# Kernel optimization log

Hardware: AMD Instinct MI355X
Metric: run time of the kernel (lower is better)

The kernel has to match this reference:

```python
import jax, jax.numpy as jnp
import numpy as np

D_MODEL = 1024
NUM_HEADS = 16
D_K = D_MODEL // NUM_HEADS
B, L = 2, 2048
NEG = -1e9


def setup_inputs() -> dict:
    key = jax.random.key(0)
    ks = jax.random.split(key, 11)
    s = 1.0 / np.sqrt(D_MODEL)
    inp = {
        "Q": jax.random.normal(ks[0], (B, L, D_MODEL), jnp.float32),
        "K": jax.random.normal(ks[1], (B, L, D_MODEL), jnp.float32),
        "V": jax.random.normal(ks[2], (B, L, D_MODEL), jnp.float32),
        # causal mask: True = valid (attend), False = masked
        "mask": jnp.tril(jnp.ones((L, L), bool))[None, None],
        # torch nn.Linear weights stored [out, in]
        "Wq": jax.random.normal(ks[3], (D_MODEL, D_MODEL), jnp.float32) * s,
        "bq": jnp.zeros((D_MODEL,), jnp.float32),
        "Wk": jax.random.normal(ks[4], (D_MODEL, D_MODEL), jnp.float32) * s,
        "bk": jnp.zeros((D_MODEL,), jnp.float32),
        "Wv": jax.random.normal(ks[5], (D_MODEL, D_MODEL), jnp.float32) * s,
        "bv": jnp.zeros((D_MODEL,), jnp.float32),
        "Wo": jax.random.normal(ks[6], (D_MODEL, D_MODEL), jnp.float32) * s,
        "bo": jnp.zeros((D_MODEL,), jnp.float32),
    }
    return inp


def _split_heads(x):  # [B,L,D] -> [B,H,L,d_k]
    b, l, _ = x.shape
    return x.reshape(b, l, NUM_HEADS, D_K).transpose(0, 2, 1, 3)


def reference(Q, K, V, mask, Wq, bq, Wk, bk, Wv, bv, Wo, bo):
    # linear projections (torch Linear: x @ W.T + b)
    q = _split_heads(Q @ Wq.T + bq)
    k = _split_heads(K @ Wk.T + bk)
    v = _split_heads(V @ Wv.T + bv)
    scores = jnp.einsum("bhqd,bhkd->bhqk", q, k) / jnp.sqrt(jnp.float32(D_K))
    scores = jnp.where(mask, scores, NEG)
    probs = jax.nn.softmax(scores, axis=-1)  # dropout inactive at inference
    attn = jnp.einsum("bhqk,bhkd->bhqd", probs, v)
    b, h, l, dk = attn.shape
    o_in = attn.transpose(0, 2, 1, 3).reshape(b, l, D_MODEL)
    return o_in @ Wo.T + bo
```

## Files before the change

kernel.cpp:

```cpp
#include <hip/hip_runtime.h>
#include <stdint.h>

#define D_MODEL 1024
#define NH 16
#define DK 64
#define BBATCH 2
#define LL 2048
#define SCALE_LOG2E 0.1803368801111244f

typedef unsigned short bfu;
typedef __attribute__((ext_vector_type(8))) short bf16x8;
typedef __attribute__((ext_vector_type(4))) float f32x4;

union BF8 { uint32_t w[4]; bf16x8 v; };

__device__ __forceinline__ bfu f2bf(float f) {
    union { float f; uint32_t u; } a; a.f = f;
    uint32_t r = a.u + 0x7FFF + ((a.u >> 16) & 1);
    return (bfu)(r >> 16);
}
__device__ __forceinline__ uint32_t pktrunc(float hi, float lo) {
    return __builtin_amdgcn_perm(__float_as_uint(hi), __float_as_uint(lo), 0x07060302);
}

__device__ __forceinline__ void gload_lds16(const void* g, void* l) {
    __builtin_amdgcn_global_load_lds(
        (const __attribute__((address_space(1))) void*)g,
        (__attribute__((address_space(3))) void*)l, 16, 0, 0);
}

__global__ __launch_bounds__(256) void cvt_all(
    const float4* __restrict__ s0, const float4* __restrict__ s1, const float4* __restrict__ s2,
    const float4* __restrict__ s3, const float4* __restrict__ s4, const float4* __restrict__ s5,
    const float4* __restrict__ s6, ushort4* __restrict__ dst)
{
    int i = blockIdx.x * 256 + threadIdx.x;
    const float4* s; int off;
    float sc = 1.0f;
    if (i < (3 << 20)) {
        int t = i >> 20; s = (t == 0) ? s0 : ((t == 1) ? s1 : s2);
        off = i & ((1 << 20) - 1);
    } else {
        int j = i - (3 << 20);
        int t = j >> 18; s = (t == 0) ? s3 : ((t == 1) ? s4 : ((t == 2) ? s5 : s6));
        if (t == 0) sc = SCALE_LOG2E;
        off = j & ((1 << 18) - 1);
    }
    float4 v = s[off];
    ushort4 o;
    o.x = f2bf(v.x * sc); o.y = f2bf(v.y * sc); o.z = f2bf(v.z * sc); o.w = f2bf(v.w * sc);
    dst[i] = o;
}

#define BM 128
#define BN 128
#define BKK 64

__device__ __forceinline__ int kperm(int k) {
    return (((k >> 4) & 1) << 5) | (((k >> 2) & 3) << 3) | (((k >> 5) & 1) << 2) | (k & 3);
}

__global__ __launch_bounds__(256, 2) void gemm_proj(
    const bfu* __restrict__ Qb, const bfu* __restrict__ Kb, const bfu* __restrict__ Vb,
    const bfu* __restrict__ Wq, const bfu* __restrict__ Wk, const bfu* __restrict__ Wv,
    const float* __restrict__ bq, const float* __restrict__ bk, const float* __restrict__ bv,
    bfu* __restrict__ qp, bfu* __restrict__ kp, bfu* __restrict__ vt)
{
    const int z = blockIdx.z;
    const bfu* A = (z == 0) ? Qb : ((z == 1) ? Kb : Vb);
    const bfu* B = (z == 0) ? Wq : ((z == 1) ? Wk : Wv);
    const float* bias = (z == 0) ? bq : ((z == 1) ? bk : bv);
    const float bsc = (z == 0) ? SCALE_LOG2E : 1.0f;
    bfu* out = (z == 0) ? qp : ((z == 1) ? kp : vt);

    __shared__ __align__(16) bfu As[BM * BKK];
    __shared__ __align__(16) bfu Bs[BN * BKK];

    const int t = threadIdx.x;
    const int lane = t & 63;
    const int wave = t >> 6;
    const int wm = wave & 1, wn = wave >> 1;
    const int tm = blockIdx.y * BM, tn = blockIdx.x * BN;
    const int lr = lane & 15, quad = lane >> 4, q8 = quad << 3;

    f32x4 acc[4][4];
    for (int i = 0; i < 4; i++) for (int j = 0; j < 4; j++) acc[i][j] = (f32x4){0.f, 0.f, 0.f, 0.f};

    for (int kt = 0; kt < 1024; kt += BKK) {
        for (int it = 0; it < 4; ++it) {
            int c = t + it * 256;
            int row = c >> 3, col = (c & 7) << 3;
            gload_lds16(&A[(size_t)(tm + row) * 1024 + kt + col], &As[(size_t)c * 8]);
        }
        for (int it = 0; it < 4; ++it) {
            int c = t + it * 256;
            int row = c >> 3, col = (c & 7) << 3;
            gload_lds16(&B[(size_t)(tn + row) * 1024 + kt + col], &Bs[(size_t)c * 8]);
        }
        __syncthreads();
        for (int ks = 0; ks < BKK; ks += 32) {
            bf16x8 a[4], b[4];
            for (int i = 0; i < 4; i++)
                a[i] = *(const bf16x8*)&As[(wm * 64 + i * 16 + lr) * BKK + ks + q8];
            for (int i = 0; i < 4; i++)
                b[i] = *(const bf16x8*)&Bs[(wn * 64 + i * 16 + lr) * BKK + ks + q8];
            for (int mt = 0; mt < 4; mt++)
                for (int nt = 0; nt < 4; nt++)
                    acc[mt][nt] = __builtin_amdgcn_mfma_f32_16x16x32_bf16(a[mt], b[nt], acc[mt][nt], 0, 0, 0);
        }
        __syncthreads();
    }

    for (int mt = 0; mt < 4; mt++)
        for (int nt = 0; nt < 4; nt++)
            for (int r = 0; r < 4; r++) {
                int m = tm + wm * 64 + mt * 16 + quad * 4 + r;
                int n = tn + wn * 64 + nt * 16 + lr;
                float v = acc[mt][nt][r] + bias[n] * bsc;
                int b_ = m >> 11, l = m & 2047;
                int h = n >> 6, d = n & 63;
                if (z < 2)
                    out[((size_t)((b_ * NH + h) * LL + l)) * DK + d] = f2bf(v);
                else {
                    int lp = (l & ~63) | kperm(l & 63);
                    out[((size_t)((b_ * NH + h) * DK + d)) * LL + lp] = f2bf(v);
                }
            }
}

__global__ __launch_bounds__(256) void attn_kernel(
    const bfu* __restrict__ qp, const bfu* __restrict__ kp, const bfu* __restrict__ vtp,
    bfu* __restrict__ attn)
{
    const int id = blockIdx.x;
    const int bh = (id & 7) | ((id >> 7) << 3);
    const int band = 15 - ((id >> 3) & 15);
    const int b_ = bh >> 4, h = bh & 15;
    const int t = threadIdx.x;
    const int lane = t & 63, w = t >> 6;
    const int lr = lane & 15, quad = lane >> 4, q8 = quad << 3;

    __shared__ __align__(16) bfu Ks[2][64 * 64];
    __shared__ __align__(16) bfu Vs[2][64 * 64];

    const int r0 = band * 128 + w * 32;
    const int jmax_b = 2 * band + 1;
    const int jmax_w = r0 >> 6;

    const bfu* kbase = kp + (size_t)bh * LL * DK;
    const bfu* vbase = vtp + (size_t)bh * DK * LL;

    bf16x8 aq[2][2];
    for (int mt = 0; mt < 2; mt++)
        for (int kx = 0; kx < 2; kx++)
            aq[mt][kx] = *(const bf16x8*)&qp[((size_t)bh * LL + r0 + mt * 16 + lr) * DK + kx * 32 + q8];

    f32x4 o[2][4];
    for (int mt = 0; mt < 2; mt++)
        for (int nf = 0; nf < 4; nf++) o[mt][nf] = (f32x4){0.f, 0.f, 0.f, 0.f};
    float lsum[2] = {0.f, 0.f};

    {
        for (int it = 0; it < 2; ++it) {
            int c = t + it * 256;
            gload_lds16(&kbase[(size_t)(0 * 64 + (c >> 3)) * DK + (c & 7) * 8], &Ks[0][(size_t)c * 8]);
        }
        for (int it = 0; it < 2; ++it) {
            int c = t + it * 256;
            gload_lds16(&vbase[(size_t)(c >> 3) * LL + 0 * 64 + (c & 7) * 8], &Vs[0][(size_t)c * 8]);
        }
    }
    __syncthreads();

    for (int j = 0; j <= jmax_b; ++j) {
        const int buf = j & 1;
        if (j < jmax_b) {
            const int nb = buf ^ 1, jn = j + 1;
            for (int it = 0; it < 2; ++it) {
                int c = t + it * 256;
                gload_lds16(&kbase[(size_t)(jn * 64 + (c >> 3)) * DK + (c & 7) * 8], &Ks[nb][(size_t)c * 8]);
            }
            for (int it = 0; it < 2; ++it) {
                int c = t + it * 256;
                gload_lds16(&vbase[(size_t)(c >> 3) * LL + jn * 64 + (c & 7) * 8], &Vs[nb][(size_t)c * 8]);
            }
        }
        if (j <= jmax_w) {
            f32x4 sv[4][2];
            for (int kt = 0; kt < 4; kt++)
                for (int mt = 0; mt < 2; mt++) sv[kt][mt] = (f32x4){0.f, 0.f, 0.f, 0.f};
            for (int kx = 0; kx < 2; kx++)
                for (int kt = 0; kt < 4; kt++) {
                    bf16x8 ak = *(const bf16x8*)&Ks[buf][(kt * 16 + lr) * 64 + kx * 32 + q8];
                    for (int mt = 0; mt < 2; mt++)
                        sv[kt][mt] = __builtin_amdgcn_mfma_f32_16x16x32_bf16(ak, aq[mt][kx], sv[kt][mt], 0, 0, 0);
                }
            if (j == jmax_w) {
                const int mb = r0 & 63;
                for (int kt = 0; kt < 4; kt++)
                    for (int mt = 0; mt < 2; mt++)
                        for (int r = 0; r < 4; r++) {
                            int kl = kt * 16 + quad * 4 + r;
                            int ml = mb + mt * 16 + lr;
                            if (kl > ml) sv[kt][mt][r] = -1e9f;
                        }
            }
            for (int kt = 0; kt < 4; kt++)
                for (int mt = 0; mt < 2; mt++)
                    for (int r = 0; r < 4; r++) {
                        float e = __builtin_amdgcn_exp2f(sv[kt][mt][r]);
                        sv[kt][mt][r] = e;
                        lsum[mt] += e;
                    }
            for (int kx = 0; kx < 2; kx++) {
                BF8 pf[2];
                for (int mt = 0; mt < 2; mt++) {
                    pf[mt].w[0] = pktrunc(sv[kx][mt][1], sv[kx][mt][0]);
                    pf[mt].w[1] = pktrunc(sv[kx][mt][3], sv[kx][mt][2]);
                    pf[mt].w[2] = pktrunc(sv[2 + kx][mt][1], sv[2 + kx][mt][0]);
                    pf[mt].w[3] = pktrunc(sv[2 + kx][mt][3], sv[2 + kx][mt][2]);
                }
                for (int nf = 0; nf < 4; nf++) {
                    bf16x8 av = *(const bf16x8*)&Vs[buf][(nf * 16 + lr) * 64 + kx * 32 + q8];
                    for (int mt = 0; mt < 2; mt++)
                        o[mt][nf] = __builtin_amdgcn_mfma_f32_16x16x32_bf16(av, pf[mt].v, o[mt][nf], 0, 0, 0);
                }
            }
        }
        __syncthreads();
    }

    for (int mt = 0; mt < 2; mt++) {
        float l = lsum[mt];
        l += __shfl_xor(l, 16);
        l += __shfl_xor(l, 32);
        float rinv = 1.0f / l;
        for (int nf = 0; nf < 4; nf++) {
            uint32_t w0 = ((uint32_t)f2bf(o[mt][nf][1] * rinv) << 16) | f2bf(o[mt][nf][0] * rinv);
            uint32_t w1 = ((uint32_t)f2bf(o[mt][nf][3] * rinv) << 16) | f2bf(o[mt][nf][2] * rinv);
            uint2 pk2 = {w0, w1};
            *(uint2*)&attn[((size_t)(b_ * LL + r0 + mt * 16 + lr)) * D_MODEL + h * DK + nf * 16 + quad * 4] = pk2;
        }
    }
}

#define OBM 128
#define OBN 64

__global__ __launch_bounds__(256) void gemm_out(
    const bfu* __restrict__ A, const bfu* __restrict__ B,
    const float* __restrict__ bias, float* __restrict__ out)
{
    __shared__ __align__(16) bfu As[OBM * 64];
    __shared__ __align__(16) bfu Bs[OBN * 64];

    const int t = threadIdx.x;
    const int lane = t & 63, w = t >> 6;
    const int tm = blockIdx.y * OBM, tn = blockIdx.x * OBN;
    const int lr = lane & 15, quad = lane >> 4, q8 = quad << 3;

    f32x4 acc[2][4];
    for (int i = 0; i < 2; i++) for (int j = 0; j < 4; j++) acc[i][j] = (f32x4){0.f, 0.f, 0.f, 0.f};

    for (int kt = 0; kt < 1024; kt += 64) {
        for (int it = 0; it < 4; ++it) {
            int c = t + it * 256;
            gload_lds16(&A[(size_t)(tm + (c >> 3)) * 1024 + kt + ((c & 7) << 3)], &As[(size_t)c * 8]);
        }
        for (int it = 0; it < 2; ++it) {
            int c = t + it * 256;
            gload_lds16(&B[(size_t)(tn + (c >> 3)) * 1024 + kt + ((c & 7) << 3)], &Bs[(size_t)c * 8]);
        }
        __syncthreads();
        for (int ks = 0; ks < 64; ks += 32) {
            bf16x8 a[2], b[4];
            for (int mt = 0; mt < 2; mt++)
                a[mt] = *(const bf16x8*)&As[(w * 32 + mt * 16 + lr) * 64 + ks + q8];
            for (int nt = 0; nt < 4; nt++)
                b[nt] = *(const bf16x8*)&Bs[(nt * 16 + lr) * 64 + ks + q8];
            for (int mt = 0; mt < 2; mt++)
                for (int nt = 0; nt < 4; nt++)
                    acc[mt][nt] = __builtin_amdgcn_mfma_f32_16x16x32_bf16(a[mt], b[nt], acc[mt][nt], 0, 0, 0);
        }
        __syncthreads();
    }

    for (int mt = 0; mt < 2; mt++)
        for (int nt = 0; nt < 4; nt++)
            for (int r = 0; r < 4; r++) {
                int m = tm + w * 32 + mt * 16 + quad * 4 + r;
                int n = tn + nt * 16 + lr;
                out[(size_t)m * D_MODEL + n] = acc[mt][nt][r] + bias[n];
            }
}

extern "C" void kernel_launch(void* const* d_in, const int* in_sizes, int n_in,
                              void* d_out, int out_size, void* d_ws, size_t ws_size,
                              hipStream_t stream) {
    const float* Q  = (const float*)d_in[0];
    const float* K  = (const float*)d_in[1];
    const float* V  = (const float*)d_in[2];
    const float* Wq = (const float*)d_in[4];
    const float* bq = (const float*)d_in[5];
    const float* Wk = (const float*)d_in[6];
    const float* bk = (const float*)d_in[7];
    const float* Wv = (const float*)d_in[8];
    const float* bv = (const float*)d_in[9];
    const float* Wo = (const float*)d_in[10];
    const float* bo = (const float*)d_in[11];
    float* out = (float*)d_out;

    char* ws = (char*)d_ws;
    bfu* Qb  = (bfu*)(ws + ((size_t)0  << 20));
    bfu* Kb  = (bfu*)(ws + ((size_t)8  << 20));
    bfu* Vb  = (bfu*)(ws + ((size_t)16 << 20));
    bfu* Wqb = (bfu*)(ws + ((size_t)24 << 20));
    bfu* Wkb = (bfu*)(ws + ((size_t)26 << 20));
    bfu* Wvb = (bfu*)(ws + ((size_t)28 << 20));
    bfu* Wob = (bfu*)(ws + ((size_t)30 << 20));
    bfu* qp  = (bfu*)(ws + ((size_t)32 << 20));
    bfu* kp  = (bfu*)(ws + ((size_t)40 << 20));
    bfu* vt  = (bfu*)(ws + ((size_t)48 << 20));
    bfu* attn = (bfu*)(ws + ((size_t)56 << 20));

    cvt_all<<<16384, 256, 0, stream>>>(
        (const float4*)Q, (const float4*)K, (const float4*)V,
        (const float4*)Wq, (const float4*)Wk, (const float4*)Wv, (const float4*)Wo,
        (ushort4*)Qb);

    gemm_proj<<<dim3(8, 32, 3), 256, 0, stream>>>(Qb, Kb, Vb, Wqb, Wkb, Wvb,
                                                  bq, bk, bv, qp, kp, vt);

    attn_kernel<<<dim3(512), 256, 0, stream>>>(qp, kp, vt, attn);

    gemm_out<<<dim3(16, 32), 256, 0, stream>>>(attn, Wob, bo, out);
}
```

Measured before the change: 243.2 us.

## Swizzle LDS tiles to avoid bank conflicts and shrink attention blocks to 64 rows

All three matmul kernels now store 16-byte chunks into LDS with an XOR swizzle on the column group (row & 7) and read them back through a matching swz() index. This is meant to remove bank conflicts on the MFMA operand reads. The attention kernel moves from 256-thread blocks covering 128 query rows to 128-thread blocks covering 64 rows, with a launch bound of 4 blocks per CU and twice as many blocks. That drops the per-wave causal skip logic, evens out causal load balance and raises occupancy, at the cost of loading each K/V tile into LDS twice as often per query row.

```diff
diff --git a/kernel.cpp b/kernel.cpp
--- a/kernel.cpp
+++ b/kernel.cpp
@@ -27,6 +27,10 @@
     __builtin_amdgcn_global_load_lds(
         (const __attribute__((address_space(1))) void*)g,
         (__attribute__((address_space(3))) void*)l, 16, 0, 0);
+}
+
+__device__ __forceinline__ int swz(int R, int G) {
+    return R * 64 + (((G ^ (R & 7))) << 3);
 }
 
 __global__ __launch_bounds__(256) void cvt_all(
@@ -81,7 +85,7 @@
     const int wave = t >> 6;
     const int wm = wave & 1, wn = wave >> 1;
     const int tm = blockIdx.y * BM, tn = blockIdx.x * BN;
-    const int lr = lane & 15, quad = lane >> 4, q8 = quad << 3;
+    const int lr = lane & 15, quad = lane >> 4;
 
     f32x4 acc[4][4];
     for (int i = 0; i < 4; i++) for (int j = 0; j < 4; j++) acc[i][j] = (f32x4){0.f, 0.f, 0.f, 0.f};
@@ -89,21 +93,21 @@
     for (int kt = 0; kt < 1024; kt += BKK) {
         for (int it = 0; it < 4; ++it) {
             int c = t + it * 256;
-            int row = c >> 3, col = (c & 7) << 3;
-            gload_lds16(&A[(size_t)(tm + row) * 1024 + kt + col], &As[(size_t)c * 8]);
+            int row = c >> 3, gx = (c & 7) ^ (row & 7);
+            gload_lds16(&A[(size_t)(tm + row) * 1024 + kt + gx * 8], &As[(size_t)c * 8]);
         }
         for (int it = 0; it < 4; ++it) {
             int c = t + it * 256;
-            int row = c >> 3, col = (c & 7) << 3;
-            gload_lds16(&B[(size_t)(tn + row) * 1024 + kt + col], &Bs[(size_t)c * 8]);
-        }
-        __syncthreads();
-        for (int ks = 0; ks < BKK; ks += 32) {
+            int row = c >> 3, gx = (c & 7) ^ (row & 7);
+            gload_lds16(&B[(size_t)(tn + row) * 1024 + kt + gx * 8], &Bs[(size_t)c * 8]);
+        }
+        __syncthreads();
+        for (int kx = 0; kx < 2; kx++) {
             bf16x8 a[4], b[4];
             for (int i = 0; i < 4; i++)
-                a[i] = *(const bf16x8*)&As[(wm * 64 + i * 16 + lr) * BKK + ks + q8];
+                a[i] = *(const bf16x8*)&As[swz(wm * 64 + i * 16 + lr, kx * 4 + quad)];
             for (int i = 0; i < 4; i++)
-                b[i] = *(const bf16x8*)&Bs[(wn * 64 + i * 16 + lr) * BKK + ks + q8];
+                b[i] = *(const bf16x8*)&Bs[swz(wn * 64 + i * 16 + lr, kx * 4 + quad)];
             for (int mt = 0; mt < 4; mt++)
                 for (int nt = 0; nt < 4; nt++)
                     acc[mt][nt] = __builtin_amdgcn_mfma_f32_16x16x32_bf16(a[mt], b[nt], acc[mt][nt], 0, 0, 0);
@@ -128,13 +132,13 @@
             }
 }
 
-__global__ __launch_bounds__(256) void attn_kernel(
+__global__ __launch_bounds__(128, 4) void attn_kernel(
     const bfu* __restrict__ qp, const bfu* __restrict__ kp, const bfu* __restrict__ vtp,
     bfu* __restrict__ attn)
 {
     const int id = blockIdx.x;
-    const int bh = (id & 7) | ((id >> 7) << 3);
-    const int band = 15 - ((id >> 3) & 15);
+    const int bh = (id & 7) | (((id >> 3) & 3) << 3);
+    const int band = 31 - (id >> 5);
     const int b_ = bh >> 4, h = bh & 15;
     const int t = threadIdx.x;
     const int lane = t & 63, w = t >> 6;
@@ -143,9 +147,8 @@
     __shared__ __align__(16) bfu Ks[2][64 * 64];
     __shared__ __align__(16) bfu Vs[2][64 * 64];
 
-    const int r0 = band * 128 + w * 32;
-    const int jmax_b = 2 * band + 1;
-    const int jmax_w = r0 >> 6;
+    const int r0 = band * 64 + w * 32;
+    const int jmax = band;
 
     const bfu* kbase = kp + (size_t)bh * LL * DK;
     const bfu* vbase = vtp + (size_t)bh * DK * LL;
@@ -160,71 +163,63 @@
         for (int nf = 0; nf < 4; nf++) o[mt][nf] = (f32x4){0.f, 0.f, 0.f, 0.f};
     float lsum[2] = {0.f, 0.f};
 
-    {
-        for (int it = 0; it < 2; ++it) {
-            int c = t + it * 256;
-            gload_lds16(&kbase[(size_t)(0 * 64 + (c >> 3)) * DK + (c & 7) * 8], &Ks[0][(size_t)c * 8]);
-        }
-        for (int it = 0; it < 2; ++it) {
-            int c = t + it * 256;
-            gload_lds16(&vbase[(size_t)(c >> 3) * LL + 0 * 64 + (c & 7) * 8], &Vs[0][(size_t)c * 8]);
-        }
+    for (int it = 0; it < 4; ++it) {
+        int c = t + it * 128;
+        int r = c >> 3, gx = (c & 7) ^ (r & 7);
+        gload_lds16(&kbase[(size_t)r * DK + gx * 8], &Ks[0][(size_t)c * 8]);
+        gload_lds16(&vbase[(size_t)r * LL + gx * 8], &Vs[0][(size_t)c * 8]);
     }
     __syncthreads();
 
-    for (int j = 0; j <= jmax_b; ++j) {
+    for (int j = 0; j <= jmax; ++j) {
         const int buf = j & 1;
-        if (j < jmax_b) {
+        if (j < jmax) {
             const int nb = buf ^ 1, jn = j + 1;
-            for (int it = 0; it < 2; ++it) {
-                int c = t + it * 256;
-                gload_lds16(&kbase[(size_t)(jn * 64 + (c >> 3)) * DK + (c & 7) * 8], &Ks[nb][(size_t)c * 8]);
-            }
-            for (int it = 0; it < 2; ++it) {
-                int c = t + it * 256;
-                gload_lds16(&vbase[(size_t)(c >> 3) * LL + jn * 64 + (c & 7) * 8], &Vs[nb][(size_t)c * 8]);
-            }
-        }
-        if (j <= jmax_w) {
-            f32x4 sv[4][2];
-            for (int kt = 0; kt < 4; kt++)
-                for (int mt = 0; mt < 2; mt++) sv[kt][mt] = (f32x4){0.f, 0.f, 0.f, 0.f};
-            for (int kx = 0; kx < 2; kx++)
-                for (int kt = 0; kt < 4; kt++) {
-                    bf16x8 ak = *(const bf16x8*)&Ks[buf][(kt * 16 + lr) * 64 + kx * 32 + q8];
-                    for (int mt = 0; mt < 2; mt++)
-                        sv[kt][mt] = __builtin_amdgcn_mfma_f32_16x16x32_bf16(ak, aq[mt][kx], sv[kt][mt], 0, 0, 0);
-                }
-            if (j == jmax_w) {
-                const int mb = r0 & 63;
-                for (int kt = 0; kt < 4; kt++)
-                    for (int mt = 0; mt < 2; mt++)
-                        for (int r = 0; r < 4; r++) {
-                            int kl = kt * 16 + quad * 4 + r;
-                            int ml = mb + mt * 16 + lr;
-                            if (kl > ml) sv[kt][mt][r] = -1e9f;
-                        }
-            }
+            for (int it = 0; it < 4; ++it) {
+                int c = t + it * 128;
+                int r = c >> 3, gx = (c & 7) ^ (r & 7);
+                gload_lds16(&kbase[(size_t)(jn * 64 + r) * DK + gx * 8], &Ks[nb][(size_t)c * 8]);
+                gload_lds16(&vbase[(size_t)r * LL + jn * 64 + gx * 8], &Vs[nb][(size_t)c * 8]);
+            }
+        }
+        f32x4 sv[4][2];
+        for (int kt = 0; kt < 4; kt++)
+            for (int mt = 0; mt < 2; mt++) sv[kt][mt] = (f32x4){0.f, 0.f, 0.f, 0.f};
+        for (int kx = 0; kx < 2; kx++)
+            for (int kt = 0; kt < 4; kt++) {
+                bf16x8 ak = *(const bf16x8*)&Ks[buf][swz(kt * 16 + lr, kx * 4 + quad)];
+                for (int mt = 0; mt < 2; mt++)
+                    sv[kt][mt] = __builtin_amdgcn_mfma_f32_16x16x32_bf16(ak, aq[mt][kx], sv[kt][mt], 0, 0, 0);
+            }
+        if (j == jmax) {
+            const int mb = r0 & 63;
             for (int kt = 0; kt < 4; kt++)
                 for (int mt = 0; mt < 2; mt++)
                     for (int r = 0; r < 4; r++) {
-                        float e = __builtin_amdgcn_exp2f(sv[kt][mt][r]);
-                        sv[kt][mt][r] = e;
-                        lsum[mt] += e;
+                        int kl = kt * 16 + quad * 4 + r;
+                        int ml = mb + mt * 16 + lr;
+                        if (kl > ml) sv[kt][mt][r] = -1e9f;
                     }
-            for (int kx = 0; kx < 2; kx++) {
-                BF8 pf[2];
-                for (int mt = 0; mt < 2; mt++) {
-                    pf[mt].w[0] = pktrunc(sv[kx][mt][1], sv[kx][mt][0]);
-                    pf[mt].w[1] = pktrunc(sv[kx][mt][3], sv[kx][mt][2]);
-                    pf[mt].w[2] = pktrunc(sv[2 + kx][mt][1], sv[2 + kx][mt][0]);
-                    pf[mt].w[3] = pktrunc(sv[2 + kx][mt][3], sv[2 + kx][mt][2]);
+        }
+        for (int kt = 0; kt < 4; kt++)
+            for (int mt = 0; mt < 2; mt++)
+                for (int r = 0; r < 4; r++) {
+                    float e = __builtin_amdgcn_exp2f(sv[kt][mt][r]);
+                    sv[kt][mt][r] = e;
+                    lsum[mt] += e;
                 }
-                for (int nf = 0; nf < 4; nf++) {
-                    bf16x8 av = *(const bf16x8*)&Vs[buf][(nf * 16 + lr) * 64 + kx * 32 + q8];
-                    for (int mt = 0; mt < 2; mt++)
-                        o[mt][nf] = __builtin_amdgcn_mfma_f32_16x16x32_bf16(av, pf[mt].v, o[mt][nf], 0, 0, 0);
-                }
+        for (int kx = 0; kx < 2; kx++) {
+            BF8 pf[2];
+            for (int mt = 0; mt < 2; mt++) {
+                pf[mt].w[0] = pktrunc(sv[kx][mt][1], sv[kx][mt][0]);
+                pf[mt].w[1] = pktrunc(sv[kx][mt][3], sv[kx][mt][2]);
+                pf[mt].w[2] = pktrunc(sv[2 + kx][mt][1], sv[2 + kx][mt][0]);
+                pf[mt].w[3] = pktrunc(sv[2 + kx][mt][3], sv[2 + kx][mt][2]);
+            }
+            for (int nf = 0; nf < 4; nf++) {
+                bf16x8 av = *(const bf16x8*)&Vs[buf][swz(nf * 16 + lr, kx * 4 + quad)];
+                for (int mt = 0; mt < 2; mt++)
+                    o[mt][nf] = __builtin_amdgcn_mfma_f32_16x16x32_bf16(av, pf[mt].v, o[mt][nf], 0, 0, 0);
             }
         }
         __syncthreads();
@@ -257,7 +252,7 @@
     const int t = threadIdx.x;
     const int lane = t & 63, w = t >> 6;
     const int tm = blockIdx.y * OBM, tn = blockIdx.x * OBN;
-    const int lr = lane & 15, quad = lane >> 4, q8 = quad << 3;
+    const int lr = lane & 15, quad = lane >> 4;
 
     f32x4 acc[2][4];
     for (int i = 0; i < 2; i++) for (int j = 0; j < 4; j++) acc[i][j] = (f32x4){0.f, 0.f, 0.f, 0.f};
@@ -265,19 +260,21 @@
     for (int kt = 0; kt < 1024; kt += 64) {
         for (int it = 0; it < 4; ++it) {
             int c = t + it * 256;
-            gload_lds16(&A[(size_t)(tm + (c >> 3)) * 1024 + kt + ((c & 7) << 3)], &As[(size_t)c * 8]);
+            int row = c >> 3, gx = (c & 7) ^ (row & 7);
+            gload_lds16(&A[(size_t)(tm + row) * 1024 + kt + gx * 8], &As[(size_t)c * 8]);
         }
         for (int it = 0; it < 2; ++it) {
             int c = t + it * 256;
-            gload_lds16(&B[(size_t)(tn + (c >> 3)) * 1024 + kt + ((c & 7) << 3)], &Bs[(size_t)c * 8]);
-        }
-        __syncthreads();
-        for (int ks = 0; ks < 64; ks += 32) {
+            int row = c >> 3, gx = (c & 7) ^ (row & 7);
+            gload_lds16(&B[(size_t)(tn + row) * 1024 + kt + gx * 8], &Bs[(size_t)c * 8]);
+        }
+        __syncthreads();
+        for (int kx = 0; kx < 2; kx++) {
             bf16x8 a[2], b[4];
             for (int mt = 0; mt < 2; mt++)
-                a[mt] = *(const bf16x8*)&As[(w * 32 + mt * 16 + lr) * 64 + ks + q8];
+                a[mt] = *(const bf16x8*)&As[swz(w * 32 + mt * 16 + lr, kx * 4 + quad)];
             for (int nt = 0; nt < 4; nt++)
-                b[nt] = *(const bf16x8*)&Bs[(nt * 16 + lr) * 64 + ks + q8];
+                b[nt] = *(const bf16x8*)&Bs[swz(nt * 16 + lr, kx * 4 + quad)];
             for (int mt = 0; mt < 2; mt++)
                 for (int nt = 0; nt < 4; nt++)
                     acc[mt][nt] = __builtin_amdgcn_mfma_f32_16x16x32_bf16(a[mt], b[nt], acc[mt][nt], 0, 0, 0);
@@ -331,7 +328,7 @@
     gemm_proj<<<dim3(8, 32, 3), 256, 0, stream>>>(Qb, Kb, Vb, Wqb, Wkb, Wvb,
                                                   bq, bk, bv, qp, kp, vt);
 
-    attn_kernel<<<dim3(512), 256, 0, stream>>>(qp, kp, vt, attn);
+    attn_kernel<<<dim3(1024), 128, 0, stream>>>(qp, kp, vt, attn);
 
     gemm_out<<<dim3(16, 32), 256, 0, stream>>>(attn, Wob, bo, out);
 }
```

Measured after the change: 232.3 us. 1.05x faster.
